# Performance work log

Hardware: AMD Instinct MI355X
Metric: run time of the kernel (lower is better)

The kernel has to match this reference:

```python
import jax, jax.numpy as jnp
import numpy as np
import math

B, N, C, H, CH = 1, 256, 128, 4, 32  # batch, n_res, pair channels, heads, head dim
LN_EPS = 1e-5


def setup_inputs() -> dict:
    key = jax.random.key(0)
    ks = jax.random.split(key, 12)
    s = 0.02
    return {
        "act": jax.random.normal(ks[0], (B, N, N, C), dtype=jnp.float32),
        "mask": (jax.random.uniform(ks[1], (B, N, N)) < 0.9).astype(jnp.float32),
        "ln_g": jnp.ones((C,), jnp.float32),
        "ln_b": jnp.zeros((C,), jnp.float32),
        "wq": jax.random.normal(ks[2], (C, H * CH), jnp.float32) * s,
        "wk": jax.random.normal(ks[3], (C, H * CH), jnp.float32) * s,
        "wv": jax.random.normal(ks[4], (C, H * CH), jnp.float32) * s,
        "w2d": jax.random.normal(ks[5], (C, H), jnp.float32) * s,
        "wg": jax.random.normal(ks[6], (C, H * CH), jnp.float32) * s,
        "bg": jnp.ones((H * CH,), jnp.float32),
        "wo": jax.random.normal(ks[7], (H * CH, C), jnp.float32) * s,
        "bo": jnp.zeros((C,), jnp.float32),
    }


def reference(act, mask, ln_g, ln_b, wq, wk, wv, w2d, wg, bg, wo, bo):
    # swap the two residue axes: attend along the *starting* node axis
    x = jnp.swapaxes(act, -2, -3)          # [b, m, i, C]
    m = jnp.swapaxes(mask, -1, -2)         # [b, m, i]
    # LayerNorm
    mu = jnp.mean(x, axis=-1, keepdims=True)
    var = jnp.var(x, axis=-1, keepdims=True)
    x = (x - mu) * jax.lax.rsqrt(var + LN_EPS) * ln_g + ln_b
    # additive mask bias: [b, m, 1, 1, i]
    bias = (1e9 * (m - 1.0))[..., :, None, None, :]
    shp = x.shape[:-1]
    q = (x @ wq).reshape(*shp, H, CH)
    k = (x @ wk).reshape(*shp, H, CH)
    v = (x @ wv).reshape(*shp, H, CH)
    factor = 1.0 / math.sqrt(CH)
    aff = jnp.einsum('bmihc,bmjhc->bmhij', q * factor, k) + bias
    # non-batched pair bias: [b, h, m, i]; broadcasts against [b, m, h, i, j]
    # exactly as in the torch code (requires b == 1)
    nb = jnp.transpose(x @ w2d, (0, 3, 1, 2))
    weights = jax.nn.softmax(aff + nb, axis=-1)  # [b, m, h, i, j]
    g = jax.nn.sigmoid((x @ wg + bg).reshape(*shp, H, CH))
    out = jnp.einsum('bmhqk,bmkhc->bmqhc', weights, v) * g
    out = out.reshape(*shp, H * CH) @ wo + bo
    return jnp.swapaxes(out, -2, -3)
```

## Files before the change

### kernel.cpp

```cpp
#include <hip/hip_runtime.h>
#include <hip/hip_bf16.h>
#include <math.h>


typedef __attribute__((ext_vector_type(8))) short short8;
typedef __attribute__((ext_vector_type(4))) short short4v;
typedef __attribute__((ext_vector_type(4))) float f32x4;

__device__ __forceinline__ unsigned short f2bf(float f) {
  __hip_bfloat16 b = __float2bfloat16(f);
  return __builtin_bit_cast(unsigned short, b);
}
__device__ __forceinline__ float bf2f(unsigned short u) {
  return __uint_as_float(((unsigned int)u) << 16);
}

__device__ __forceinline__ f32x4 mfma16(short8 a, short8 b, f32x4 c) {
  return __builtin_amdgcn_mfma_f32_16x16x32_bf16(a, b, c, 0, 0, 0);
}

__global__ __launch_bounds__(256) void k_ln(const float* __restrict__ act,
                                            const float* __restrict__ ln_g,
                                            const float* __restrict__ ln_b,
                                            const float* __restrict__ wq,
                                            const float* __restrict__ wk,
                                            const float* __restrict__ wv,
                                            const float* __restrict__ wg,
                                            const float* __restrict__ w2d,
                                            const float* __restrict__ wo,
                                            const float* __restrict__ mask,
                                            unsigned short* __restrict__ lnxb,
                                            unsigned short* __restrict__ Wt4,
                                            unsigned short* __restrict__ Wto,
                                            float* __restrict__ maskT) {
  int t = threadIdx.x;
  if (blockIdx.x >= 4096) {
    int idx = (blockIdx.x - 4096) * 256 + t;
    if (idx < 65536) {
      int n = idx >> 7, k = idx & 127;
      const float* ws = (n < 128) ? wq : (n < 256) ? wk : (n < 384) ? wv : wg;
      Wt4[idx] = f2bf(ws[k * 128 + (n & 127)]);
    } else if (idx < 73728) {
      int j = idx - 65536;
      int r = j >> 7, k = j & 127;
      Wt4[idx] = (r < 4) ? f2bf(w2d[k * 4 + r]) : (unsigned short)0;
    } else if (idx < 90112) {
      int j = idx - 73728;
      int n = j >> 7, k = j & 127;
      Wto[j] = f2bf(wo[k * 128 + n]);
    } else if (idx < 155648) {
      int j2 = idx - 90112;
      int mi = j2 & 255, jj = j2 >> 8;
      maskT[mi * 256 + jj] = 1e9f * (mask[jj * 256 + mi] - 1.0f);
    }
    return;
  }
  int grp = t >> 4, l16 = t & 15;
  int row = blockIdx.x * 16 + grp;
  int mm = row >> 8, ii = row & 255;
  const float4* a = (const float4*)(act + ((size_t)(ii * 256 + mm)) * 128);
  float4 v0 = a[l16 * 2], v1 = a[l16 * 2 + 1];
  float s = (v0.x + v0.y) + (v0.z + v0.w) + (v1.x + v1.y) + (v1.z + v1.w);
  #pragma unroll
  for (int off = 1; off < 16; off <<= 1) s += __shfl_xor(s, off, 64);
  float mean = s * (1.f / 128.f);
  float e[8] = {v0.x - mean, v0.y - mean, v0.z - mean, v0.w - mean,
                v1.x - mean, v1.y - mean, v1.z - mean, v1.w - mean};
  float vs = (e[0]*e[0] + e[1]*e[1]) + (e[2]*e[2] + e[3]*e[3]) +
             (e[4]*e[4] + e[5]*e[5]) + (e[6]*e[6] + e[7]*e[7]);
  #pragma unroll
  for (int off = 1; off < 16; off <<= 1) vs += __shfl_xor(vs, off, 64);
  float rstd = rsqrtf(vs * (1.f / 128.f) + 1e-5f);
  const float4* gp = (const float4*)ln_g;
  const float4* bp = (const float4*)ln_b;
  float4 g0 = gp[l16 * 2], g1 = gp[l16 * 2 + 1];
  float4 b0 = bp[l16 * 2], b1 = bp[l16 * 2 + 1];
  short8 o;
  o[0] = (short)f2bf(e[0] * rstd * g0.x + b0.x);
  o[1] = (short)f2bf(e[1] * rstd * g0.y + b0.y);
  o[2] = (short)f2bf(e[2] * rstd * g0.z + b0.z);
  o[3] = (short)f2bf(e[3] * rstd * g0.w + b0.w);
  o[4] = (short)f2bf(e[4] * rstd * g1.x + b1.x);
  o[5] = (short)f2bf(e[5] * rstd * g1.y + b1.y);
  o[6] = (short)f2bf(e[6] * rstd * g1.z + b1.z);
  o[7] = (short)f2bf(e[7] * rstd * g1.w + b1.w);
  *(short8*)(lnxb + (size_t)row * 128 + l16 * 8) = o;
}

__global__ __launch_bounds__(256) void k_projg(const unsigned short* __restrict__ A,
                                               const unsigned short* __restrict__ Bt,
                                               const float* __restrict__ bg,
                                               unsigned short* __restrict__ qb,
                                               unsigned short* __restrict__ kb,
                                               unsigned short* __restrict__ vb,
                                               unsigned short* __restrict__ sgb,
                                               float* __restrict__ b2t) {
  __shared__ unsigned short As[128 * 136];
  int t = threadIdx.x;
  int m0 = blockIdx.x * 128;
  int w = t >> 6, l = t & 63, g = l >> 4, li = l & 15;
  int wr = w >> 1, wc = w & 1;
  {
    int row = t >> 1, c0 = (t & 1) * 64;
    const unsigned short* src = A + (size_t)(m0 + row) * 128 + c0;
    #pragma unroll
    for (int k8 = 0; k8 < 8; ++k8)
      *(short8*)&As[row * 136 + c0 + k8 * 8] = *(const short8*)(src + k8 * 8);
  }
  __syncthreads();
  const float factor = 0.17677669529663687f;
  for (int nb = 0; nb < 9; ++nb) {
    int n0 = nb * 64;
    f32x4 acc[4][2] = {};
    #pragma unroll
    for (int s = 0; s < 4; ++s) {
      int k0 = s * 32;
      short8 af[4], bf[2];
      #pragma unroll
      for (int it = 0; it < 4; ++it)
        af[it] = *(const short8*)&As[(wr * 64 + it * 16 + li) * 136 + k0 + g * 8];
      #pragma unroll
      for (int jt = 0; jt < 2; ++jt)
        bf[jt] = *(const short8*)(Bt + (size_t)(n0 + wc * 32 + jt * 16 + li) * 128 + k0 + g * 8);
      #pragma unroll
      for (int it = 0; it < 4; ++it)
        #pragma unroll
        for (int jt = 0; jt < 2; ++jt)
          acc[it][jt] = mfma16(bf[jt], af[it], acc[it][jt]);
    }
    int which = n0 >> 7;
    if (which == 4) {
      if (wc == 0 && g == 0) {
        #pragma unroll
        for (int it = 0; it < 4; ++it) {
          int R = m0 + wr * 64 + it * 16 + li;
          int mm = R >> 8, ii = R & 255;
          #pragma unroll
          for (int r = 0; r < 4; ++r)
            b2t[(size_t)r * 65536 + ii * 256 + mm] = acc[it][0][r];
        }
      }
      continue;
    }
    #pragma unroll
    for (int it = 0; it < 4; ++it) {
      int R = m0 + wr * 64 + it * 16 + li;
      int mm = R >> 8, ii = R & 255;
      #pragma unroll
      for (int jt = 0; jt < 2; ++jt) {
        int nb4 = n0 + wc * 32 + jt * 16 + g * 4;
        int hh = (nb4 >> 5) & 3, ch = nb4 & 31;
        size_t o = ((size_t)((mm * 4 + hh) * 256 + ii)) * 32 + ch;
        short4v pk;
        if (which == 0) {
          #pragma unroll
          for (int r = 0; r < 4; ++r) pk[r] = (short)f2bf(acc[it][jt][r] * factor);
          *(short4v*)(qb + o) = pk;
        } else if (which == 1) {
          #pragma unroll
          for (int r = 0; r < 4; ++r) pk[r] = (short)f2bf(acc[it][jt][r]);
          *(short4v*)(kb + o) = pk;
        } else if (which == 2) {
          #pragma unroll
          for (int r = 0; r < 4; ++r) pk[r] = (short)f2bf(acc[it][jt][r]);
          *(short4v*)(vb + o) = pk;
        } else {
          #pragma unroll
          for (int r = 0; r < 4; ++r)
            pk[r] = (short)f2bf(1.f / (1.f + __expf(-(acc[it][jt][r] + bg[(nb4 & 127) + r]))));
          *(short4v*)(sgb + o) = pk;
        }
      }
    }
  }
}

__global__ __launch_bounds__(256) void k_attn(const unsigned short* __restrict__ qb,
                                              const unsigned short* __restrict__ kb,
                                              const unsigned short* __restrict__ vb,
                                              const unsigned short* __restrict__ sgb,
                                              const float* __restrict__ b2t,
                                              const float* __restrict__ maskT,
                                              unsigned short* __restrict__ aob) {
  __shared__ unsigned short VT[32 * 264];
  __shared__ unsigned short Pl[4 * 32 * 72];
  __shared__ float maskls[256];
  int m = blockIdx.x >> 1, ihalf = blockIdx.x & 1, h = blockIdx.y;
  int t = threadIdx.x, w = t >> 6, l = t & 63, g = l >> 4, li = l & 15;
  int base = (m * 4 + h) << 8;
  maskls[t] = maskT[m * 256 + t];
  {
    const unsigned int* v32 = (const unsigned int*)(vb + (size_t)base * 32);
    #pragma unroll
    for (int p = 0; p < 16; ++p) {
      int idx = t + p * 256;
      int j = idx >> 4, cp = idx & 15;
      unsigned int u = v32[idx];
      VT[(cp * 2) * 264 + j]     = (unsigned short)(u & 0xffff);
      VT[(cp * 2 + 1) * 264 + j] = (unsigned short)(u >> 16);
    }
  }
  __syncthreads();
  int i0 = ihalf * 128 + w * 32;
  short8 qf[2];
  #pragma unroll
  for (int it = 0; it < 2; ++it)
    qf[it] = *(const short8*)(qb + ((size_t)(base + i0 + it * 16 + li)) * 32 + g * 8);
  float mst[2] = {-1e30f, -1e30f};
  float lst[2] = {0.f, 0.f};
  f32x4 oacc[2][2] = {};
  const float* b2 = b2t + (size_t)h * 65536;
  unsigned short* Pw = Pl + w * 32 * 72;
  for (int jc = 0; jc < 4; ++jc) {
    int j0 = jc * 64;
    f32x4 sacc[4][2];
    #pragma unroll
    for (int jt = 0; jt < 4; ++jt) {
      short8 kf = *(const short8*)(kb + ((size_t)(base + j0 + jt * 16 + li)) * 32 + g * 8);
      #pragma unroll
      for (int it = 0; it < 2; ++it) {
        f32x4 z = {0.f, 0.f, 0.f, 0.f};
        sacc[jt][it] = mfma16(kf, qf[it], z);
      }
    }
    #pragma unroll
    for (int it = 0; it < 2; ++it) {
      int ic = i0 + it * 16 + li;
      float s[16];
      float cmax = -1e30f;
      #pragma unroll
      for (int jt = 0; jt < 4; ++jt) {
        int jb = j0 + jt * 16 + g * 4;
        f32x4 mk = *(const f32x4*)&maskls[jb];
        #pragma unroll
        for (int r = 0; r < 4; ++r) {
          float sv = sacc[jt][it][r] + b2[(size_t)(jb + r) * 256 + ic] + mk[r];
          s[jt * 4 + r] = sv;
          cmax = fmaxf(cmax, sv);
        }
      }
      cmax = fmaxf(cmax, __shfl_xor(cmax, 16));
      cmax = fmaxf(cmax, __shfl_xor(cmax, 32));
      float mnew = fmaxf(mst[it], cmax);
      float fac = __expf(mst[it] - mnew);
      mst[it] = mnew;
      lst[it] *= fac;
      oacc[0][it] *= fac;
      oacc[1][it] *= fac;
      float psum = 0.f;
      #pragma unroll
      for (int jt = 0; jt < 4; ++jt) {
        float p0 = __expf(s[jt * 4 + 0] - mnew);
        float p1 = __expf(s[jt * 4 + 1] - mnew);
        float p2 = __expf(s[jt * 4 + 2] - mnew);
        float p3 = __expf(s[jt * 4 + 3] - mnew);
        psum += p0 + p1 + p2 + p3;
        short4v pk;
        pk.x = (short)f2bf(p0); pk.y = (short)f2bf(p1);
        pk.z = (short)f2bf(p2); pk.w = (short)f2bf(p3);
        *(short4v*)&Pw[(it * 16 + li) * 72 + jt * 16 + g * 4] = pk;
      }
      lst[it] += psum;
    }
    asm volatile("" ::: "memory");
    #pragma unroll
    for (int ks = 0; ks < 2; ++ks) {
      short8 vf0 = *(const short8*)&VT[li * 264        + j0 + ks * 32 + g * 8];
      short8 vf1 = *(const short8*)&VT[(16 + li) * 264 + j0 + ks * 32 + g * 8];
      #pragma unroll
      for (int it = 0; it < 2; ++it) {
        short8 pf = *(const short8*)&Pw[(it * 16 + li) * 72 + ks * 32 + g * 8];
        oacc[0][it] = mfma16(vf0, pf, oacc[0][it]);
        oacc[1][it] = mfma16(vf1, pf, oacc[1][it]);
      }
    }
    asm volatile("" ::: "memory");
  }
  #pragma unroll
  for (int it = 0; it < 2; ++it) {
    float lt = lst[it];
    lt += __shfl_xor(lt, 16);
    lt += __shfl_xor(lt, 32);
    float inv = 1.f / lt;
    int ic = i0 + it * 16 + li;
    #pragma unroll
    for (int ct = 0; ct < 2; ++ct) {
      int c0 = ct * 16 + g * 4;
      const unsigned short* grow = sgb + ((size_t)(base + ic)) * 32 + c0;
      ushort4 gu = *(const ushort4*)grow;
      ushort4 ov;
      ov.x = f2bf(oacc[ct][it][0] * inv * bf2f(gu.x));
      ov.y = f2bf(oacc[ct][it][1] * inv * bf2f(gu.y));
      ov.z = f2bf(oacc[ct][it][2] * inv * bf2f(gu.z));
      ov.w = f2bf(oacc[ct][it][3] * inv * bf2f(gu.w));
      *(ushort4*)&aob[((size_t)(ic * 256 + m)) * 128 + h * 32 + c0] = ov;
    }
  }
}

__global__ __launch_bounds__(256) void k_outg(const unsigned short* __restrict__ A,
                                              const unsigned short* __restrict__ Bt,
                                              const float* __restrict__ bo,
                                              float* __restrict__ out) {
  __shared__ unsigned short As[128 * 136];
  int t = threadIdx.x;
  int m0 = blockIdx.x * 128;
  int w = t >> 6, l = t & 63, g = l >> 4, li = l & 15;
  int wr = w >> 1, wc = w & 1;
  {
    int row = t >> 1, c0 = (t & 1) * 64;
    const unsigned short* src = A + (size_t)(m0 + row) * 128 + c0;
    #pragma unroll
    for (int k8 = 0; k8 < 8; ++k8)
      *(short8*)&As[row * 136 + c0 + k8 * 8] = *(const short8*)(src + k8 * 8);
  }
  __syncthreads();
  #pragma unroll
  for (int nb = 0; nb < 2; ++nb) {
    int n0 = nb * 64;
    f32x4 acc[4][2] = {};
    #pragma unroll
    for (int s = 0; s < 4; ++s) {
      int k0 = s * 32;
      short8 af[4], bf[2];
      #pragma unroll
      for (int it = 0; it < 4; ++it)
        af[it] = *(const short8*)&As[(wr * 64 + it * 16 + li) * 136 + k0 + g * 8];
      #pragma unroll
      for (int jt = 0; jt < 2; ++jt)
        bf[jt] = *(const short8*)(Bt + (size_t)(n0 + wc * 32 + jt * 16 + li) * 128 + k0 + g * 8);
      #pragma unroll
      for (int it = 0; it < 4; ++it)
        #pragma unroll
        for (int jt = 0; jt < 2; ++jt)
          acc[it][jt] = mfma16(bf[jt], af[it], acc[it][jt]);
    }
    #pragma unroll
    for (int it = 0; it < 4; ++it) {
      int R = m0 + wr * 64 + it * 16 + li;
      #pragma unroll
      for (int jt = 0; jt < 2; ++jt) {
        int nb4 = n0 + wc * 32 + jt * 16 + g * 4;
        float4 o;
        o.x = acc[it][jt][0] + bo[nb4 + 0];
        o.y = acc[it][jt][1] + bo[nb4 + 1];
        o.z = acc[it][jt][2] + bo[nb4 + 2];
        o.w = acc[it][jt][3] + bo[nb4 + 3];
        *(float4*)(out + (size_t)R * 128 + nb4) = o;
      }
    }
  }
}

extern "C" void kernel_launch(void* const* d_in, const int* in_sizes, int n_in,
                              void* d_out, int out_size, void* d_ws, size_t ws_size,
                              hipStream_t stream) {
  const float* act  = (const float*)d_in[0];
  const float* mask = (const float*)d_in[1];
  const float* ln_g = (const float*)d_in[2];
  const float* ln_b = (const float*)d_in[3];
  const float* wq   = (const float*)d_in[4];
  const float* wk   = (const float*)d_in[5];
  const float* wv   = (const float*)d_in[6];
  const float* w2d  = (const float*)d_in[7];
  const float* wg   = (const float*)d_in[8];
  const float* bg   = (const float*)d_in[9];
  const float* wo   = (const float*)d_in[10];
  const float* bo   = (const float*)d_in[11];

  char* p = (char*)d_ws;
  unsigned short* lnxb  = (unsigned short*)p;  p += (size_t)8388608 * 2;
  float*          b2t   = (float*)p;           p += (size_t)262144 * 4;
  unsigned short* qb    = (unsigned short*)p;  p += (size_t)8388608 * 2;
  unsigned short* kb    = (unsigned short*)p;  p += (size_t)8388608 * 2;
  unsigned short* vb    = (unsigned short*)p;  p += (size_t)8388608 * 2;
  unsigned short* sgb   = (unsigned short*)p;  p += (size_t)8388608 * 2;
  unsigned short* aob   = (unsigned short*)p;  p += (size_t)8388608 * 2;
  unsigned short* Wt4   = (unsigned short*)p;  p += (size_t)73728 * 2;
  unsigned short* Wto   = (unsigned short*)p;  p += (size_t)16384 * 2;
  float*          maskT = (float*)p;           p += (size_t)65536 * 4;
  float* out = (float*)d_out;

  hipLaunchKernelGGL(k_ln,    dim3(4704),   dim3(256), 0, stream,
                     act, ln_g, ln_b, wq, wk, wv, wg, w2d, wo, mask, lnxb, Wt4, Wto, maskT);
  hipLaunchKernelGGL(k_projg, dim3(512),    dim3(256), 0, stream, lnxb, Wt4, bg, qb, kb, vb, sgb, b2t);
  hipLaunchKernelGGL(k_attn,  dim3(512, 4), dim3(256), 0, stream, qb, kb, vb, sgb, b2t, maskT, aob);
  hipLaunchKernelGGL(k_outg,  dim3(512),    dim3(256), 0, stream, aob, Wto, bo, out);
}
```

Measured before the change: 104.0 us.

## Split projection and output GEMMs across N-tiles via 2D grids

The projection GEMM kernel now splits its 9 output column tiles across 3 blockIdx.y slices, so the grid grows from 512 to 1536 blocks. The output GEMM splits its 2 column tiles across blockIdx.y and now stages both the A and B K-slices in shared memory, using smaller padded tiles instead of loading the full A row block once. Both changes aim to expose more blocks for parallelism and occupancy on a device with many CUs. The cost is that the A tile is reloaded by several blocks, and the output kernel adds extra barriers per K step.

```diff
diff --git a/kernel.cpp b/kernel.cpp
--- a/kernel.cpp
+++ b/kernel.cpp
@@ -109,7 +109,9 @@
   }
   __syncthreads();
   const float factor = 0.17677669529663687f;
-  for (int nb = 0; nb < 9; ++nb) {
+  #pragma unroll
+  for (int nbi = 0; nbi < 3; ++nbi) {
+    int nb = blockIdx.y * 3 + nbi;
     int n0 = nb * 64;
     f32x4 acc[4][2] = {};
     #pragma unroll
@@ -302,52 +304,50 @@
                                               const unsigned short* __restrict__ Bt,
                                               const float* __restrict__ bo,
                                               float* __restrict__ out) {
-  __shared__ unsigned short As[128 * 136];
+  __shared__ unsigned short As[128 * 40];
+  __shared__ unsigned short Bs[64 * 40];
   int t = threadIdx.x;
-  int m0 = blockIdx.x * 128;
+  int m0 = blockIdx.x * 128, n0 = blockIdx.y * 64;
   int w = t >> 6, l = t & 63, g = l >> 4, li = l & 15;
   int wr = w >> 1, wc = w & 1;
-  {
-    int row = t >> 1, c0 = (t & 1) * 64;
-    const unsigned short* src = A + (size_t)(m0 + row) * 128 + c0;
-    #pragma unroll
-    for (int k8 = 0; k8 < 8; ++k8)
-      *(short8*)&As[row * 136 + c0 + k8 * 8] = *(const short8*)(src + k8 * 8);
-  }
-  __syncthreads();
-  #pragma unroll
-  for (int nb = 0; nb < 2; ++nb) {
-    int n0 = nb * 64;
-    f32x4 acc[4][2] = {};
-    #pragma unroll
-    for (int s = 0; s < 4; ++s) {
-      int k0 = s * 32;
-      short8 af[4], bf[2];
-      #pragma unroll
-      for (int it = 0; it < 4; ++it)
-        af[it] = *(const short8*)&As[(wr * 64 + it * 16 + li) * 136 + k0 + g * 8];
+  f32x4 acc[4][2] = {};
+  for (int s = 0; s < 4; ++s) {
+    int k0 = s * 32;
+    __syncthreads();
+    {
+      int row = t >> 1, kl = (t & 1) * 16;
+      const short8* src = (const short8*)(A + (size_t)(m0 + row) * 128 + k0 + kl);
+      *(short8*)&As[row * 40 + kl]     = src[0];
+      *(short8*)&As[row * 40 + kl + 8] = src[1];
+      int bn = t >> 2, bk = (t & 3) * 8;
+      *(short8*)&Bs[bn * 40 + bk] = *(const short8*)(Bt + (size_t)(n0 + bn) * 128 + k0 + bk);
+    }
+    __syncthreads();
+    short8 af[4], bf[2];
+    #pragma unroll
+    for (int it = 0; it < 4; ++it)
+      af[it] = *(const short8*)&As[(wr * 64 + it * 16 + li) * 40 + g * 8];
+    #pragma unroll
+    for (int jt = 0; jt < 2; ++jt)
+      bf[jt] = *(const short8*)&Bs[(wc * 32 + jt * 16 + li) * 40 + g * 8];
+    #pragma unroll
+    for (int it = 0; it < 4; ++it)
       #pragma unroll
       for (int jt = 0; jt < 2; ++jt)
-        bf[jt] = *(const short8*)(Bt + (size_t)(n0 + wc * 32 + jt * 16 + li) * 128 + k0 + g * 8);
-      #pragma unroll
-      for (int it = 0; it < 4; ++it)
-        #pragma unroll
-        for (int jt = 0; jt < 2; ++jt)
-          acc[it][jt] = mfma16(bf[jt], af[it], acc[it][jt]);
-    }
-    #pragma unroll
-    for (int it = 0; it < 4; ++it) {
-      int R = m0 + wr * 64 + it * 16 + li;
-      #pragma unroll
-      for (int jt = 0; jt < 2; ++jt) {
-        int nb4 = n0 + wc * 32 + jt * 16 + g * 4;
-        float4 o;
-        o.x = acc[it][jt][0] + bo[nb4 + 0];
-        o.y = acc[it][jt][1] + bo[nb4 + 1];
-        o.z = acc[it][jt][2] + bo[nb4 + 2];
-        o.w = acc[it][jt][3] + bo[nb4 + 3];
-        *(float4*)(out + (size_t)R * 128 + nb4) = o;
-      }
+        acc[it][jt] = mfma16(bf[jt], af[it], acc[it][jt]);
+  }
+  #pragma unroll
+  for (int it = 0; it < 4; ++it) {
+    int R = m0 + wr * 64 + it * 16 + li;
+    #pragma unroll
+    for (int jt = 0; jt < 2; ++jt) {
+      int nb4 = n0 + wc * 32 + jt * 16 + g * 4;
+      float4 o;
+      o.x = acc[it][jt][0] + bo[nb4 + 0];
+      o.y = acc[it][jt][1] + bo[nb4 + 1];
+      o.z = acc[it][jt][2] + bo[nb4 + 2];
+      o.w = acc[it][jt][3] + bo[nb4 + 3];
+      *(float4*)(out + (size_t)R * 128 + nb4) = o;
     }
   }
 }
@@ -383,7 +383,7 @@
 
   hipLaunchKernelGGL(k_ln,    dim3(4704),   dim3(256), 0, stream,
                      act, ln_g, ln_b, wq, wk, wv, wg, w2d, wo, mask, lnxb, Wt4, Wto, maskT);
-  hipLaunchKernelGGL(k_projg, dim3(512),    dim3(256), 0, stream, lnxb, Wt4, bg, qb, kb, vb, sgb, b2t);
+  hipLaunchKernelGGL(k_projg, dim3(512, 3), dim3(256), 0, stream, lnxb, Wt4, bg, qb, kb, vb, sgb, b2t);
   hipLaunchKernelGGL(k_attn,  dim3(512, 4), dim3(256), 0, stream, qb, kb, vb, sgb, b2t, maskT, aob);
-  hipLaunchKernelGGL(k_outg,  dim3(512),    dim3(256), 0, stream, aob, Wto, bo, out);
-}
+  hipLaunchKernelGGL(k_outg,  dim3(512, 2), dim3(256), 0, stream, aob, Wto, bo, out);
+}
```

Result: no change. 102.9 us (-1.1%).
